# Kernel tuning notes

Measured on AMD Instinct MI355X. Metric: run time of the kernel, lower is better.

The kernel has to match this reference:

```python
import jax, jax.numpy as jnp
import numpy as np

ALPHA = 0.2  # LeakyReLU negative slope (init arg `alpha`)
NEG_INF = -9e15  # matches torch's -9000000000000000.0 fill
D_Q = 128
D_V = 128


def setup_inputs() -> dict:
    key = jax.random.key(0)
    k1, k2, k3, k4, k5 = jax.random.split(key, 5)
    B, N = 8, 256
    query = jax.random.normal(k1, (B, N * N, D_Q), dtype=jnp.float32)
    value = jax.random.normal(k2, (B, N * N, D_V), dtype=jnp.float32)
    mask = jax.random.randint(k3, (B, N, N), 0, 2, dtype=jnp.int32)
    # nn.Linear(d_q + d_v, 1): weight flattened to a (d_q+d_v,) vector, scalar bias
    W = jax.random.normal(k4, (D_Q + D_V,), dtype=jnp.float32) * (1.0 / np.sqrt(D_Q + D_V))
    b = jax.random.normal(k5, (1,), dtype=jnp.float32) * 0.01
    return {"query": query, "value": value, "mask": mask, "W": W, "b": b}


def reference(query, value, mask, W, b):
    B, NN, dq = query.shape
    N = int(NN ** 0.5)
    dv = value.shape[-1]
    q = query.reshape(-1, N, dq)          # [B*N, N, d_q]
    v = value.reshape(-1, N, dv)          # [B*N, N, d_v]
    # cat([q, v], -1) @ W + b  ==  q @ W[:dq] + v @ W[dq:] + b  (avoids concat alloc)
    energy = (jnp.einsum('bnd,d->bn', q, W[:dq])
              + jnp.einsum('bnd,d->bn', v, W[dq:]) + b[0])  # [B*N, N]
    energy = jnp.where(energy >= 0, energy, ALPHA * energy)   # leaky_relu
    m = mask.reshape(-1, N)                                    # [B*N, N]
    attention = jnp.where(m > 0, energy, NEG_INF)
    scores = jax.nn.softmax(attention, axis=1)                 # dropout: identity (eval)
    out = jnp.einsum('bn,bnd->bd', scores, v)                  # bmm([B*N,1,N],[B*N,N,dv])
    return out.reshape(-1, N, dv)                              # [B, N, d_v]
```

## Files before the change

kernel.cpp:

```cpp
#include <hip/hip_runtime.h>
#include <math.h>


constexpr int NR  = 256;
constexpr int DIM = 128;
constexpr float LALPHA  = 0.2f;
constexpr float NEG_INF = -9.0e15f;

template<int CTRL>
__device__ __forceinline__ float dpp_mov(float x) {
    return __int_as_float(
        __builtin_amdgcn_update_dpp(0, __float_as_int(x), CTRL, 0xF, 0xF, true));
}

__global__ __launch_bounds__(256) void graph_attn_kernel(
    const float* __restrict__ q,
    const float* __restrict__ v,
    const int*   __restrict__ mask,
    const float* __restrict__ W,
    const float* __restrict__ bptr,
    float*       __restrict__ out)
{
    const int g    = blockIdx.x;
    const int t    = threadIdx.x;
    const int hw   = t >> 5;
    const int lane = t & 31;
    const int L    = t & 3;

    __shared__ float s_mask[NR];
    __shared__ float s_m[8], s_l[8];
    __shared__ float s_o[8][DIM];

    s_mask[t] = (mask[g * NR + t] > 0) ? 1.0f : 0.0f;
    __syncthreads();

    const float4 wq = *(const float4*)(W + lane * 4);
    const float4 wv = *(const float4*)(W + DIM + lane * 4);
    const float bias = bptr[0];

    const float* qp = q + (size_t)g * NR * DIM + (size_t)hw * 32 * DIM + lane * 4;
    const float* vp = v + (size_t)g * NR * DIM + (size_t)hw * 32 * DIM + lane * 4;

    float mrow[8];
#pragma unroll
    for (int k = 0; k < 8; ++k) mrow[k] = s_mask[(hw << 5) + (k << 2) + L];

    const bool odd1 = (t & 1) != 0;
    const bool odd2 = (t & 2) != 0;

    float m = -INFINITY;
    float l = 0.0f;
    float4 o = make_float4(0.f, 0.f, 0.f, 0.f);

    float4 Q[4], V[4];
#pragma unroll
    for (int r = 0; r < 4; ++r) {
        Q[r] = *(const float4*)(qp + r * DIM);
        V[r] = *(const float4*)(vp + r * DIM);
    }

#pragma unroll
    for (int k = 0; k < 8; ++k) {
        float4 Qn[4], Vn[4];
        if (k < 7) {
            const float* qk = qp + (k + 1) * (4 * DIM);
            const float* vk = vp + (k + 1) * (4 * DIM);
#pragma unroll
            for (int r = 0; r < 4; ++r) {
                Qn[r] = *(const float4*)(qk + r * DIM);
                Vn[r] = *(const float4*)(vk + r * DIM);
            }
        }

        float pe0 = Q[0].x*wq.x + Q[0].y*wq.y + Q[0].z*wq.z + Q[0].w*wq.w
                  + V[0].x*wv.x + V[0].y*wv.y + V[0].z*wv.z + V[0].w*wv.w;
        float pe1 = Q[1].x*wq.x + Q[1].y*wq.y + Q[1].z*wq.z + Q[1].w*wq.w
                  + V[1].x*wv.x + V[1].y*wv.y + V[1].z*wv.z + V[1].w*wv.w;
        float pe2 = Q[2].x*wq.x + Q[2].y*wq.y + Q[2].z*wq.z + Q[2].w*wq.w
                  + V[2].x*wv.x + V[2].y*wv.y + V[2].z*wv.z + V[2].w*wv.w;
        float pe3 = Q[3].x*wq.x + Q[3].y*wq.y + Q[3].z*wq.z + Q[3].w*wq.w
                  + V[3].x*wv.x + V[3].y*wv.y + V[3].z*wv.z + V[3].w*wv.w;

        float sA = (odd1 ? pe1 : pe0) + dpp_mov<0xB1>(odd1 ? pe0 : pe1);
        float sB = (odd1 ? pe3 : pe2) + dpp_mov<0xB1>(odd1 ? pe2 : pe3);
        float s  = (odd2 ? sB  : sA ) + dpp_mov<0x4E>(odd2 ? sA  : sB );
        s += dpp_mov<0x124>(s);
        s += dpp_mov<0x128>(s);
        s += __shfl_xor(s, 16);

        float e = s + bias;
        e = fmaxf(e, LALPHA * e);
        e = (mrow[k] > 0.f) ? e : NEG_INF;

        float gm = fmaxf(e, dpp_mov<0xB1>(e));
        gm = fmaxf(gm, dpp_mov<0x4E>(gm));

        const float m_new = fmaxf(m, gm);
        const float scale = __expf(m - m_new);
        const float p     = __expf(e - m_new);

        const float p0 = dpp_mov<0x00>(p);
        const float p1 = dpp_mov<0x55>(p);
        const float p2 = dpp_mov<0xAA>(p);
        const float p3 = dpp_mov<0xFF>(p);

        l = l * scale + ((p0 + p1) + (p2 + p3));
        o.x = o.x * scale + (p0*V[0].x + p1*V[1].x + p2*V[2].x + p3*V[3].x);
        o.y = o.y * scale + (p0*V[0].y + p1*V[1].y + p2*V[2].y + p3*V[3].y);
        o.z = o.z * scale + (p0*V[0].z + p1*V[1].z + p2*V[2].z + p3*V[3].z);
        o.w = o.w * scale + (p0*V[0].w + p1*V[1].w + p2*V[2].w + p3*V[3].w);
        m = m_new;

        if (k < 7) {
#pragma unroll
            for (int r = 0; r < 4; ++r) { Q[r] = Qn[r]; V[r] = Vn[r]; }
        }
    }

    if (lane == 0) { s_m[hw] = m; s_l[hw] = l; }
    *(float4*)(&s_o[hw][lane * 4]) = o;
    __syncthreads();

    if (t < DIM) {
        float M = s_m[0];
#pragma unroll
        for (int i = 1; i < 8; ++i) M = fmaxf(M, s_m[i]);
        float Ls = 0.f, O = 0.f;
#pragma unroll
        for (int i = 0; i < 8; ++i) {
            const float w = __expf(s_m[i] - M);
            Ls += w * s_l[i];
            O += w * s_o[i][t];
        }
        out[(size_t)g * DIM + t] = O / Ls;
    }
}

extern "C" void kernel_launch(void* const* d_in, const int* in_sizes, int n_in,
                              void* d_out, int out_size, void* d_ws, size_t ws_size,
                              hipStream_t stream) {
    const float* q    = (const float*)d_in[0];
    const float* v    = (const float*)d_in[1];
    const int*   mask = (const int*)d_in[2];
    const float* W    = (const float*)d_in[3];
    const float* b    = (const float*)d_in[4];
    float* out = (float*)d_out;

    const int G = in_sizes[0] / (NR * DIM);
    graph_attn_kernel<<<G, 256, 0, stream>>>(q, v, mask, W, b, out);
}
```

Baseline: 494.9 us.

## Stage Q/V tiles into LDS via async global_load_lds double buffering

Replaces per-thread register prefetch of query/value rows with block-wide asynchronous global-to-LDS copies (global_load_lds) into double-buffered 32-row tiles, then reads each thread's rows from LDS. Row assignment changes so each tile covers all half-waves, with the mask indexing remapped to match. The aim is deeper memory-level parallelism on this bandwidth-bound kernel, at the cost of 64KB of LDS per block (lower occupancy) and a __syncthreads per tile. There is no explicit wait on the async LDS loads before the barrier, which relies on the compiler inserting vmcnt waits.

```diff
diff --git a/kernel.cpp b/kernel.cpp
--- a/kernel.cpp
+++ b/kernel.cpp
@@ -2,10 +2,20 @@
 #include <math.h>
 
 
-constexpr int NR  = 256;
-constexpr int DIM = 128;
+constexpr int NR    = 256;
+constexpr int DIM   = 128;
+constexpr int TROWS = 32;
+constexpr int NT    = NR / TROWS;
 constexpr float LALPHA  = 0.2f;
 constexpr float NEG_INF = -9.0e15f;
+
+#define GLOBAL_AS __attribute__((address_space(1)))
+#define LDS_AS    __attribute__((address_space(3)))
+
+__device__ __forceinline__ void stage1k(const float* gsrc, float* lds_uniform) {
+    __builtin_amdgcn_global_load_lds((const GLOBAL_AS unsigned int*)gsrc,
+                                     (LDS_AS unsigned int*)lds_uniform, 16, 0, 0);
+}
 
 template<int CTRL>
 __device__ __forceinline__ float dpp_mov(float x) {
@@ -26,7 +36,11 @@
     const int hw   = t >> 5;
     const int lane = t & 31;
     const int L    = t & 3;
+    const int wvid = t >> 6;
+    const int wl   = t & 63;
 
+    __shared__ float bufQ[2][TROWS][DIM];
+    __shared__ float bufV[2][TROWS][DIM];
     __shared__ float s_mask[NR];
     __shared__ float s_m[8], s_l[8];
     __shared__ float s_o[8][DIM];
@@ -34,52 +48,62 @@
     s_mask[t] = (mask[g * NR + t] > 0) ? 1.0f : 0.0f;
     __syncthreads();
 
-    const float4 wq = *(const float4*)(W + lane * 4);
-    const float4 wv = *(const float4*)(W + DIM + lane * 4);
+    const float4 wq  = *(const float4*)(W + lane * 4);
+    const float4 wv4 = *(const float4*)(W + DIM + lane * 4);
     const float bias = bptr[0];
 
-    const float* qp = q + (size_t)g * NR * DIM + (size_t)hw * 32 * DIM + lane * 4;
-    const float* vp = v + (size_t)g * NR * DIM + (size_t)hw * 32 * DIM + lane * 4;
+    const float* qg = q + (size_t)g * NR * DIM;
+    const float* vg = v + (size_t)g * NR * DIM;
 
-    float mrow[8];
+    float mrow[NT];
 #pragma unroll
-    for (int k = 0; k < 8; ++k) mrow[k] = s_mask[(hw << 5) + (k << 2) + L];
+    for (int k = 0; k < NT; ++k) mrow[k] = s_mask[(k << 5) + (hw << 2) + L];
 
     const bool odd1 = (t & 1) != 0;
     const bool odd2 = (t & 2) != 0;
+
+    auto STAGE = [&](int b, int tl) {
+        const float* qt = qg + (size_t)tl * TROWS * DIM;
+        const float* vt = vg + (size_t)tl * TROWS * DIM;
+#pragma unroll
+        for (int j = 0; j < 4; ++j) {
+            const int fo = (wvid * 4 + j) * 256;
+            stage1k(qt + fo + wl * 4, &bufQ[b][0][0] + fo);
+            stage1k(vt + fo + wl * 4, &bufV[b][0][0] + fo);
+        }
+    };
 
     float m = -INFINITY;
     float l = 0.0f;
     float4 o = make_float4(0.f, 0.f, 0.f, 0.f);
 
-    float4 Q[4], V[4];
-#pragma unroll
-    for (int r = 0; r < 4; ++r) {
-        Q[r] = *(const float4*)(qp + r * DIM);
-        V[r] = *(const float4*)(vp + r * DIM);
-    }
+    STAGE(0, 0);
+    __syncthreads();
 
 #pragma unroll
-    for (int k = 0; k < 8; ++k) {
-        float4 Qn[4], Vn[4];
-        if (k < 7) {
-            const float* qk = qp + (k + 1) * (4 * DIM);
-            const float* vk = vp + (k + 1) * (4 * DIM);
-#pragma unroll
-            for (int r = 0; r < 4; ++r) {
-                Qn[r] = *(const float4*)(qk + r * DIM);
-                Vn[r] = *(const float4*)(vk + r * DIM);
-            }
-        }
+    for (int tl = 0; tl < NT; ++tl) {
+        if (tl + 1 < NT) STAGE((tl + 1) & 1, tl + 1);
 
-        float pe0 = Q[0].x*wq.x + Q[0].y*wq.y + Q[0].z*wq.z + Q[0].w*wq.w
-                  + V[0].x*wv.x + V[0].y*wv.y + V[0].z*wv.z + V[0].w*wv.w;
-        float pe1 = Q[1].x*wq.x + Q[1].y*wq.y + Q[1].z*wq.z + Q[1].w*wq.w
-                  + V[1].x*wv.x + V[1].y*wv.y + V[1].z*wv.z + V[1].w*wv.w;
-        float pe2 = Q[2].x*wq.x + Q[2].y*wq.y + Q[2].z*wq.z + Q[2].w*wq.w
-                  + V[2].x*wv.x + V[2].y*wv.y + V[2].z*wv.z + V[2].w*wv.w;
-        float pe3 = Q[3].x*wq.x + Q[3].y*wq.y + Q[3].z*wq.z + Q[3].w*wq.w
-                  + V[3].x*wv.x + V[3].y*wv.y + V[3].z*wv.z + V[3].w*wv.w;
+        const int b = tl & 1;
+        const float* bq = &bufQ[b][hw << 2][lane << 2];
+        const float* bv = &bufV[b][hw << 2][lane << 2];
+        const float4 Q0 = *(const float4*)(bq + 0 * DIM);
+        const float4 Q1 = *(const float4*)(bq + 1 * DIM);
+        const float4 Q2 = *(const float4*)(bq + 2 * DIM);
+        const float4 Q3 = *(const float4*)(bq + 3 * DIM);
+        const float4 V0 = *(const float4*)(bv + 0 * DIM);
+        const float4 V1 = *(const float4*)(bv + 1 * DIM);
+        const float4 V2 = *(const float4*)(bv + 2 * DIM);
+        const float4 V3 = *(const float4*)(bv + 3 * DIM);
+
+        float pe0 = Q0.x*wq.x + Q0.y*wq.y + Q0.z*wq.z + Q0.w*wq.w
+                  + V0.x*wv4.x + V0.y*wv4.y + V0.z*wv4.z + V0.w*wv4.w;
+        float pe1 = Q1.x*wq.x + Q1.y*wq.y + Q1.z*wq.z + Q1.w*wq.w
+                  + V1.x*wv4.x + V1.y*wv4.y + V1.z*wv4.z + V1.w*wv4.w;
+        float pe2 = Q2.x*wq.x + Q2.y*wq.y + Q2.z*wq.z + Q2.w*wq.w
+                  + V2.x*wv4.x + V2.y*wv4.y + V2.z*wv4.z + V2.w*wv4.w;
+        float pe3 = Q3.x*wq.x + Q3.y*wq.y + Q3.z*wq.z + Q3.w*wq.w
+                  + V3.x*wv4.x + V3.y*wv4.y + V3.z*wv4.z + V3.w*wv4.w;
 
         float sA = (odd1 ? pe1 : pe0) + dpp_mov<0xB1>(odd1 ? pe0 : pe1);
         float sB = (odd1 ? pe3 : pe2) + dpp_mov<0xB1>(odd1 ? pe2 : pe3);
@@ -90,7 +114,7 @@
 
         float e = s + bias;
         e = fmaxf(e, LALPHA * e);
-        e = (mrow[k] > 0.f) ? e : NEG_INF;
+        e = (mrow[tl] > 0.f) ? e : NEG_INF;
 
         float gm = fmaxf(e, dpp_mov<0xB1>(e));
         gm = fmaxf(gm, dpp_mov<0x4E>(gm));
@@ -105,16 +129,13 @@
         const float p3 = dpp_mov<0xFF>(p);
 
         l = l * scale + ((p0 + p1) + (p2 + p3));
-        o.x = o.x * scale + (p0*V[0].x + p1*V[1].x + p2*V[2].x + p3*V[3].x);
-        o.y = o.y * scale + (p0*V[0].y + p1*V[1].y + p2*V[2].y + p3*V[3].y);
-        o.z = o.z * scale + (p0*V[0].z + p1*V[1].z + p2*V[2].z + p3*V[3].z);
-        o.w = o.w * scale + (p0*V[0].w + p1*V[1].w + p2*V[2].w + p3*V[3].w);
+        o.x = o.x * scale + (p0*V0.x + p1*V1.x + p2*V2.x + p3*V3.x);
+        o.y = o.y * scale + (p0*V0.y + p1*V1.y + p2*V2.y + p3*V3.y);
+        o.z = o.z * scale + (p0*V0.z + p1*V1.z + p2*V2.z + p3*V3.z);
+        o.w = o.w * scale + (p0*V0.w + p1*V1.w + p2*V2.w + p3*V3.w);
         m = m_new;
 
-        if (k < 7) {
-#pragma unroll
-            for (int r = 0; r < 4; ++r) { Q[r] = Qn[r]; V[r] = Vn[r]; }
-        }
+        __syncthreads();
     }
 
     if (lane == 0) { s_m[hw] = m; s_l[hw] = l; }
```

Result: slower. 508.1 us (+2.7%).
